# Kernel optimization log

Measured on AMD Instinct MI355X. Metric: run time of the kernel, lower is better.

Reference implementation:

```python
import jax, jax.numpy as jnp
import numpy as np

B, S, D = 4, 2048, 1024
H = 16
DK = D // H  # 64, dim_k == dim_v
FF = 4096
EPS = 1e-5


def layer_norm(x, g, b):
    mu = jnp.mean(x, axis=-1, keepdims=True)
    var = jnp.mean(jnp.square(x - mu), axis=-1, keepdims=True)
    return (x - mu) * jax.lax.rsqrt(var + EPS) * g + b


def setup_inputs() -> dict:
    key = jax.random.key(0)
    ks = jax.random.split(key, 16)
    s = 0.02
    return {
        "src": jax.random.normal(ks[0], (B, S, D), jnp.float32),
        # per-head Q/K/V projections (stacked over heads)
        "wq": jax.random.normal(ks[1], (H, D, DK), jnp.float32) * s,
        "bq": jnp.zeros((H, DK), jnp.float32),
        "wk": jax.random.normal(ks[2], (H, D, DK), jnp.float32) * s,
        "bk": jnp.zeros((H, DK), jnp.float32),
        "wv": jax.random.normal(ks[3], (H, D, DK), jnp.float32) * s,
        "bv": jnp.zeros((H, DK), jnp.float32),
        # output projection: concat(H*DK) -> D
        "wo": jax.random.normal(ks[4], (H * DK, D), jnp.float32) * s,
        "bo": jnp.zeros((D,), jnp.float32),
        "ln1_g": jnp.ones((D,), jnp.float32),
        "ln1_b": jnp.zeros((D,), jnp.float32),
        # FFN
        "w1": jax.random.normal(ks[5], (D, FF), jnp.float32) * s,
        "b1": jnp.zeros((FF,), jnp.float32),
        "w2": jax.random.normal(ks[6], (FF, D), jnp.float32) * s,
        "b2": jnp.zeros((D,), jnp.float32),
        "ln2_g": jnp.ones((D,), jnp.float32),
        "ln2_b": jnp.zeros((D,), jnp.float32),
    }


def reference(src, wq, bq, wk, bk, wv, bv, wo, bo, ln1_g, ln1_b,
              w1, b1, w2, b2, ln2_g, ln2_b):
    # per-head projections: [B,S,D] x [H,D,K] -> [B,H,S,K]
    q = jnp.einsum('bsd,hdk->bhsk', src, wq) + bq[None, :, None, :]
    k = jnp.einsum('bsd,hdk->bhsk', src, wk) + bk[None, :, None, :]
    v = jnp.einsum('bsd,hdk->bhsk', src, wv) + bv[None, :, None, :]
    scale = 1.0 / jnp.sqrt(jnp.float32(DK))
    scores = jnp.einsum('bhsk,bhtk->bhst', q, k) * scale  # [B,H,S,S]
    attn = jax.nn.softmax(scores, axis=-1)
    o = jnp.einsum('bhst,bhtv->bhsv', attn, v)            # [B,H,S,DK]
    o = o.transpose(0, 2, 1, 3).reshape(B, S, H * DK)      # concat heads
    attn_out = o @ wo + bo
    x = layer_norm(src + attn_out, ln1_g, ln1_b)
    ff = jax.nn.relu(x @ w1 + b1) @ w2 + b2
    return layer_norm(x + ff, ln2_g, ln2_b)
```

## Files before the change

kernel.cpp:

```cpp
#include <hip/hip_runtime.h>

typedef __bf16 bf16;
typedef __bf16 bf16x8 __attribute__((ext_vector_type(8)));
typedef __bf16 bf16x4 __attribute__((ext_vector_type(4)));
typedef float  f32x4  __attribute__((ext_vector_type(4)));
typedef float  f32x16 __attribute__((ext_vector_type(16)));
typedef unsigned int u32;
typedef int i32x2 __attribute__((ext_vector_type(2)));

#define NB 4
#define NS 2048
#define ND 1024
#define NH 16
#define NDK 64
#define NFF 4096
#define NM (NB*NS)

#define QSCALE 0.18033688f

__device__ __forceinline__ void load_lds16(const void* g, void* l) {
  __builtin_amdgcn_global_load_lds(
      (const __attribute__((address_space(1))) void*)g,
      (__attribute__((address_space(3))) void*)l, 16, 0, 0);
}

__device__ __forceinline__ u32 pack2(float a, float b) {
  union { bf16 h[2]; u32 u; } z;
  z.h[0] = (bf16)a; z.h[1] = (bf16)b;
  return z.u;
}

__device__ __forceinline__ i32x2 pswap(u32 a, u32 b) {
#if __has_builtin(__builtin_amdgcn_permlane32_swap)
  return __builtin_amdgcn_permlane32_swap((int)a, (int)b, false, false);
#else
  u32 x = a, y = b;
  asm volatile("v_permlane32_swap_b32 %0, %1" : "+v"(x), "+v"(y));
  i32x2 r; r[0] = (int)x; r[1] = (int)y; return r;
#endif
}

__global__ __launch_bounds__(256)
void cvt_f32_bf16(const float* __restrict__ in, bf16* __restrict__ out, int n) {
  int i = (blockIdx.x * 256 + threadIdx.x) * 4;
  if (i < n) {
    float4 v = *(const float4*)&in[i];
    bf16x4 o;
    o[0] = (bf16)v.x; o[1] = (bf16)v.y; o[2] = (bf16)v.z; o[3] = (bf16)v.w;
    *(bf16x4*)&out[i] = o;
  }
}

__global__ __launch_bounds__(256)
void transpose_cvt(const float* __restrict__ in, bf16* __restrict__ out,
                   int R, int C, size_t in_bs, size_t out_bs) {
  __shared__ float t[32][33];
  int bx = blockIdx.x, by = blockIdx.y, bz = blockIdx.z;
  const float* ip = in + (size_t)bz * in_bs + (size_t)(bx * 32) * C + by * 32;
  bf16* op = out + (size_t)bz * out_bs + (size_t)(by * 32) * R + bx * 32;
  int x = threadIdx.x & 31, y = threadIdx.x >> 5;
#pragma unroll
  for (int yy = 0; yy < 32; yy += 8)
    t[y + yy][x] = ip[(size_t)(y + yy) * C + x];
  __syncthreads();
#pragma unroll
  for (int yy = 0; yy < 32; yy += 8)
    op[(size_t)(y + yy) * R + x] = (bf16)t[x][y + yy];
}

__global__ __launch_bounds__(256)
void transpose_v(const bf16* __restrict__ v, bf16* __restrict__ vT) {
  __shared__ bf16 t[64][72];
  int st = blockIdx.x;
  int bh = blockIdx.y;
  const bf16* ip = v + ((size_t)bh * NS + st * 64) * NDK;
  bf16* op = vT + (size_t)bh * NDK * NS + st * 64;
  int tid = threadIdx.x;
#pragma unroll
  for (int c = tid; c < 512; c += 256) {
    int r = c >> 3, q = c & 7;
    bf16x8 d = *(const bf16x8*)&ip[(size_t)r * NDK + q * 8];
#pragma unroll
    for (int j = 0; j < 8; j++) t[r][q * 8 + j] = d[j];
  }
  __syncthreads();
#pragma unroll
  for (int c = tid; c < 512; c += 256) {
    int dv = c >> 3, sq = c & 7;
    bf16x8 d;
#pragma unroll
    for (int j = 0; j < 8; j++) d[j] = t[sq * 8 + j][dv];
    *(bf16x8*)&op[(size_t)dv * NS + sq * 8] = d;
  }
}

#define BAR()  __builtin_amdgcn_s_barrier()
#define LGKM0() do { asm volatile("s_waitcnt lgkmcnt(0)" ::: "memory"); \
                     __builtin_amdgcn_sched_barrier(0); } while (0)

template<int BN, int EPI>
__global__ __launch_bounds__(512, 2)
void gemm8p(const bf16* __restrict__ A, const bf16* __restrict__ Bt,
            const float* __restrict__ bias0, const float* __restrict__ bias1,
            const float* __restrict__ bias2, void* __restrict__ out0,
            int M, int N, int K) {
  constexpr int NFR = BN / 64;
  __shared__ __align__(16) bf16 lA[2][256 * 64];
  __shared__ __align__(16) bf16 lB[2][BN * 64];

  const int tid = threadIdx.x, lane = tid & 63, w = tid >> 6;
  const int wr = w >> 2, wn = w & 3;
  const int blane = lane & 15, glane = lane >> 4;

  const int nwg = gridDim.x;
  const int cpx = nwg >> 3;
  const int bid = blockIdx.x;
  const int swzb = (bid & 7) * cpx + (bid >> 3);
  const int gridM = M >> 8;
  const int bm = (swzb % gridM) * 256;
  const int bn = (swzb / gridM) * BN;

  f32x4 acc[8][NFR] = {};
  bf16x8 aF[8], bF[2 * NFR];

  auto stageA = [&](int kt, int h, int b) {
#pragma unroll
    for (int j = 0; j < 2; j++) {
      int ch = w * 128 + j * 64 + lane;
      int r = h * 128 + (ch >> 3), s = ch & 7;
      load_lds16(A + (size_t)(bm + r) * K + kt * 64 + ((s ^ (r & 7)) * 8),
                 &lA[b][(h * 1024 + ch) * 8]);
    }
  };
  auto stageB = [&](int kt, int h, int b) {
    if constexpr (BN == 256) {
#pragma unroll
      for (int j = 0; j < 2; j++) {
        int ch = w * 128 + j * 64 + lane;
        int r = h * 128 + (ch >> 3), s = ch & 7;
        load_lds16(Bt + (size_t)(bn + r) * K + kt * 64 + ((s ^ (r & 7)) * 8),
                   &lB[b][(h * 1024 + ch) * 8]);
      }
    } else {
      int ch = w * 64 + lane;
      int r = h * 64 + (ch >> 3), s = ch & 7;
      load_lds16(Bt + (size_t)(bn + r) * K + kt * 64 + ((s ^ (r & 7)) * 8),
                 &lB[b][(h * 512 + ch) * 8]);
    }
  };
  auto vmwait = [&]() {
    if constexpr (BN == 256) asm volatile("s_waitcnt vmcnt(6)" ::: "memory");
    else                     asm volatile("s_waitcnt vmcnt(4)" ::: "memory");
  };
  auto ldA = [&](int mh, int b) {
#pragma unroll
    for (int mf = 0; mf < 4; mf++)
#pragma unroll
      for (int ks = 0; ks < 2; ks++) {
        int r = wr * 128 + mh * 64 + mf * 16 + blane;
        int s = (ks * 4 + glane) ^ (r & 7);
        aF[mf * 2 + ks] = *(const bf16x8*)&lA[b][r * 64 + s * 8];
      }
  };
  auto ldBh = [&](int nh, int b) {
#pragma unroll
    for (int nq = 0; nq < NFR / 2; nq++)
#pragma unroll
      for (int ks = 0; ks < 2; ks++) {
        int nf = nh * (NFR / 2) + nq;
        int r = wn * (NFR * 16) + nf * 16 + blane;
        int s = (ks * 4 + glane) ^ (r & 7);
        bF[nf * 2 + ks] = *(const bf16x8*)&lB[b][r * 64 + s * 8];
      }
  };

#define MMAQ(mh, nh)  do {                                                  \
    __builtin_amdgcn_s_setprio(1);                                          \
    _Pragma("unroll")                                                       \
    for (int mf = 0; mf < 4; mf++)                                          \
      _Pragma("unroll")                                                     \
      for (int nq = 0; nq < NFR / 2; nq++)                                  \
        _Pragma("unroll")                                                   \
        for (int ks = 0; ks < 2; ks++)                                      \
          acc[(mh) * 4 + mf][(nh) * (NFR / 2) + nq] =                       \
            __builtin_amdgcn_mfma_f32_16x16x32_bf16(                        \
              aF[mf * 2 + ks], bF[((nh) * (NFR / 2) + nq) * 2 + ks],        \
              acc[(mh) * 4 + mf][(nh) * (NFR / 2) + nq], 0, 0, 0);          \
    __builtin_amdgcn_s_setprio(0);                                          \
  } while (0)

  stageB(0, 0, 0); stageB(0, 1, 0); stageA(0, 0, 0); stageA(0, 1, 0);
  stageB(1, 0, 1); stageB(1, 1, 1); stageA(1, 0, 1);
  vmwait();
  BAR();

  const int NT = K >> 6;
  for (int u = 0; u < NT; u += 2) {
    const int t2 = (u + 2 < NT) ? u + 2 : u;
    const int t3 = (u + 3 < NT) ? u + 3 : u + 1;
    ldA(0, 0); ldBh(0, 0);
    stageA(u + 1, 1, 1);
    BAR(); LGKM0(); MMAQ(0, 0); BAR();
    ldBh(1, 0);
    stageB(t2, 0, 0);
    BAR(); LGKM0(); MMAQ(0, 1); BAR();
    ldA(1, 0);
    stageB(t2, 1, 0);
    BAR(); LGKM0(); MMAQ(1, 1); BAR();
    stageA(t2, 0, 0);
    BAR(); MMAQ(1, 0); vmwait(); BAR();
    ldA(0, 1); ldBh(0, 1);
    stageA(t2, 1, 0);
    BAR(); LGKM0(); MMAQ(0, 0); BAR();
    ldBh(1, 1);
    stageB(t3, 0, 1);
    BAR(); LGKM0(); MMAQ(0, 1); BAR();
    ldA(1, 1);
    stageB(t3, 1, 1);
    BAR(); LGKM0(); MMAQ(1, 1); BAR();
    stageA(t3, 0, 1);
    BAR(); MMAQ(1, 0); vmwait(); BAR();
  }

#pragma unroll
  for (int am = 0; am < 8; am++) {
#pragma unroll
    for (int nf = 0; nf < NFR; nf++) {
      int col = bn + wn * (NFR * 16) + nf * 16 + blane;
      int rowb = bm + wr * 128 + (am >> 2) * 64 + (am & 3) * 16 + glane * 4;
      if (EPI == 0) {
        int sel = col >> 10;
        int hh = (col & 1023) >> 6;
        int dv = col & 63;
        const float* bp = (sel == 0) ? bias0 : (sel == 1) ? bias1 : bias2;
        float bias = bp[col & 1023];
        float sc = (sel == 0) ? QSCALE : 1.0f;
        bf16* outb = (bf16*)out0 + (size_t)sel * NB * NH * NS * NDK;
#pragma unroll
        for (int i = 0; i < 4; i++) {
          int row = rowb + i;
          int b_ = row >> 11, s_ = row & 2047;
          outb[(((size_t)(b_ * NH + hh) * NS + s_) * NDK) + dv] = (bf16)((acc[am][nf][i] + bias) * sc);
        }
      } else if (EPI == 1) {
        float bias = bias0[col];
#pragma unroll
        for (int i = 0; i < 4; i++) {
          float v = acc[am][nf][i] + bias;
          v = v > 0.f ? v : 0.f;
          ((bf16*)out0)[(size_t)(rowb + i) * N + col] = (bf16)v;
        }
      } else {
        float bias = bias0[col];
#pragma unroll
        for (int i = 0; i < 4; i++)
          ((float*)out0)[(size_t)(rowb + i) * N + col] = acc[am][nf][i] + bias;
      }
    }
  }
#undef MMAQ
}

__global__ __launch_bounds__(256)
void flash_attn5(const bf16* __restrict__ q, const bf16* __restrict__ k,
                 const bf16* __restrict__ vT, bf16* __restrict__ o) {
  __shared__ __align__(16) bf16 lK[2][64 * 64];
  __shared__ __align__(16) bf16 lV[2][64 * 64];
  const int tid = threadIdx.x, lane = tid & 63, w = tid >> 6;
  const int ql = lane & 31, hi = lane >> 5;
  const int bh = blockIdx.y, qt = blockIdx.x;
  const size_t hb = (size_t)bh * NS * NDK;
  const int qrow = qt * 128 + w * 32 + ql;

  bf16x8 qf[4];
#pragma unroll
  for (int ks = 0; ks < 4; ks++)
    qf[ks] = *(const bf16x8*)&q[hb + (size_t)qrow * NDK + ks * 16 + hi * 8];

  const int rA = tid & 63;
  const int sA = tid >> 6;
  const bf16* kc0 = k  + hb + (size_t)rA * NDK + sA * 8;
  const bf16* kc1 = k  + hb + (size_t)rA * NDK + (sA + 4) * 8;
  const bf16* vc0 = vT + hb + (size_t)rA * NS  + sA * 8;
  const bf16* vc1 = vT + hb + (size_t)rA * NS  + (sA + 4) * 8;

  f32x16 o0 = {}, o1 = {};
  float ls0 = 0.f, ls1 = 0.f, ls2 = 0.f, ls3 = 0.f;

  load_lds16(kc0, &lK[0][tid * 8]);
  load_lds16(kc1, &lK[0][(tid + 256) * 8]);
  load_lds16(vc0, &lV[0][tid * 8]);
  load_lds16(vc1, &lV[0][(tid + 256) * 8]);
  __syncthreads();

  const char* lKc = (const char*)&lK[0][0];
  const char* lVc = (const char*)&lV[0][0];

  for (int t = 0; t < NS / 64; t++) {
    const int cur = t & 1;
    if (t < NS / 64 - 1) {
      const size_t ko = (size_t)(t + 1) * 64 * NDK;
      const int vo = (t + 1) * 64;
      load_lds16(kc0 + ko, &lK[cur ^ 1][tid * 8]);
      load_lds16(kc1 + ko, &lK[cur ^ 1][(tid + 256) * 8]);
      load_lds16(vc0 + vo, &lV[cur ^ 1][tid * 8]);
      load_lds16(vc1 + vo, &lV[cur ^ 1][(tid + 256) * 8]);
    }
    const char* Kb = lKc + cur * 8192;
    const char* Vb = lVc + cur * 8192;

    f32x16 st0 = {}, st1 = {};
    __builtin_amdgcn_s_setprio(1);
#pragma unroll
    for (int ks = 0; ks < 4; ks++) {
      const int c = 2 * ks + hi;
      bf16x8 kf0 = *(const bf16x8*)(Kb + ((c * 64 + ql) << 4));
      bf16x8 kf1 = *(const bf16x8*)(Kb + ((c * 64 + 32 + ql) << 4));
      st0 = __builtin_amdgcn_mfma_f32_32x32x16_bf16(kf0, qf[ks], st0, 0, 0, 0);
      st1 = __builtin_amdgcn_mfma_f32_32x32x16_bf16(kf1, qf[ks], st1, 0, 0, 0);
    }
    __builtin_amdgcn_s_setprio(0);

#pragma unroll
    for (int r = 0; r < 16; r += 4) {
      float p00 = exp2f(st0[r]),     p01 = exp2f(st0[r + 1]);
      float p02 = exp2f(st0[r + 2]), p03 = exp2f(st0[r + 3]);
      float p10 = exp2f(st1[r]),     p11 = exp2f(st1[r + 1]);
      float p12 = exp2f(st1[r + 2]), p13 = exp2f(st1[r + 3]);
      st0[r] = p00; st0[r + 1] = p01; st0[r + 2] = p02; st0[r + 3] = p03;
      st1[r] = p10; st1[r + 1] = p11; st1[r + 2] = p12; st1[r + 3] = p13;
      ls0 += p00 + p10; ls1 += p01 + p11;
      ls2 += p02 + p12; ls3 += p03 + p13;
    }

#pragma unroll
    for (int tt = 0; tt < 2; tt++) {
      f32x16 stv = (tt == 0) ? st0 : st1;
      u32 wv[8];
#pragma unroll
      for (int i = 0; i < 8; i++) wv[i] = pack2(stv[2 * i], stv[2 * i + 1]);
#pragma unroll
      for (int kk = 0; kk < 2; kk++) {
        const int base = 4 * kk;
        i32x2 e0 = pswap(wv[base + 0], wv[base + 2]);
        i32x2 e1 = pswap(wv[base + 1], wv[base + 3]);
        union { u32 u[4]; bf16x8 v; } pf;
        pf.u[0] = (u32)e0[0];
        pf.u[1] = (u32)e1[0];
        pf.u[2] = (u32)e0[1];
        pf.u[3] = (u32)e1[1];
        const int ks = 2 * tt + kk;
        const int c = 2 * ks + hi;
        bf16x8 vf0 = *(const bf16x8*)(Vb + ((c * 64 + ql) << 4));
        bf16x8 vf1 = *(const bf16x8*)(Vb + ((c * 64 + 32 + ql) << 4));
        __builtin_amdgcn_s_setprio(1);
        o0 = __builtin_amdgcn_mfma_f32_32x32x16_bf16(vf0, pf.v, o0, 0, 0, 0);
        o1 = __builtin_amdgcn_mfma_f32_32x32x16_bf16(vf1, pf.v, o1, 0, 0, 0);
        __builtin_amdgcn_s_setprio(0);
      }
    }
    __syncthreads();
  }

  float ls = (ls0 + ls1) + (ls2 + ls3);
  float lR;
  {
    i32x2 sr = pswap((u32)__float_as_int(ls), (u32)__float_as_int(ls));
    float lsp = __int_as_float(hi ? sr[0] : sr[1]);
    float lo_ = hi ? lsp : ls, hi_ = hi ? ls : lsp;
    lR = lo_ + hi_;
  }
  float invl = 1.0f / lR;
  int b_ = bh >> 4, h_ = bh & 15;
  bf16* ob = o + ((size_t)(b_ * NS + qrow) * (NH * NDK)) + h_ * NDK;
#pragma unroll
  for (int rp = 0; rp < 8; rp++) {
    int dv = 8 * (rp >> 1) + 2 * (rp & 1) + 4 * hi;
    *(u32*)&ob[dv]      = pack2(o0[2 * rp] * invl, o0[2 * rp + 1] * invl);
    *(u32*)&ob[dv + 32] = pack2(o1[2 * rp] * invl, o1[2 * rp + 1] * invl);
  }
}

template<int WB>
__global__ __launch_bounds__(256)
void ln_res(const float* __restrict__ a, const float* __restrict__ b,
            const float* __restrict__ g, const float* __restrict__ be,
            float* __restrict__ y, bf16* __restrict__ yb) {
  int row = blockIdx.x;
  int tid = threadIdx.x;
  const float4* a4 = (const float4*)(a + (size_t)row * ND);
  const float4* b4 = (const float4*)(b + (size_t)row * ND);
  float4 av = a4[tid], bv = b4[tid];
  float x0 = av.x + bv.x, x1 = av.y + bv.y, x2 = av.z + bv.z, x3 = av.w + bv.w;
  float s = x0 + x1 + x2 + x3;
  float qq_ = x0 * x0 + x1 * x1 + x2 * x2 + x3 * x3;
#pragma unroll
  for (int d = 1; d < 64; d <<= 1) { s += __shfl_xor(s, d); qq_ += __shfl_xor(qq_, d); }
  __shared__ float ss[4], sq[4];
  int w = tid >> 6, lane = tid & 63;
  if (lane == 0) { ss[w] = s; sq[w] = qq_; }
  __syncthreads();
  s = ss[0] + ss[1] + ss[2] + ss[3];
  qq_ = sq[0] + sq[1] + sq[2] + sq[3];
  float mu = s * (1.0f / ND);
  float var = qq_ * (1.0f / ND) - mu * mu;
  float rs = 1.0f / sqrtf(var + 1e-5f);
  const float4* g4 = (const float4*)g;
  const float4* e4 = (const float4*)be;
  float4 gv = g4[tid], ev = e4[tid];
  float o0 = (x0 - mu) * rs * gv.x + ev.x;
  float o1 = (x1 - mu) * rs * gv.y + ev.y;
  float o2 = (x2 - mu) * rs * gv.z + ev.z;
  float o3 = (x3 - mu) * rs * gv.w + ev.w;
  float4 ov = {o0, o1, o2, o3};
  *(float4*)(y + (size_t)row * ND + tid * 4) = ov;
  if (WB) {
    bf16x4 wv;
    wv[0] = (bf16)o0; wv[1] = (bf16)o1; wv[2] = (bf16)o2; wv[3] = (bf16)o3;
    *(bf16x4*)&yb[(size_t)row * ND + tid * 4] = wv;
  }
}

extern "C" void kernel_launch(void* const* d_in, const int* in_sizes, int n_in,
                              void* d_out, int out_size, void* d_ws, size_t ws_size,
                              hipStream_t stream) {
  const float* src = (const float*)d_in[0];
  const float* wq  = (const float*)d_in[1];
  const float* bq  = (const float*)d_in[2];
  const float* wk  = (const float*)d_in[3];
  const float* bk  = (const float*)d_in[4];
  const float* wv  = (const float*)d_in[5];
  const float* bv  = (const float*)d_in[6];
  const float* wo  = (const float*)d_in[7];
  const float* bo  = (const float*)d_in[8];
  const float* g1  = (const float*)d_in[9];
  const float* be1 = (const float*)d_in[10];
  const float* w1  = (const float*)d_in[11];
  const float* b1  = (const float*)d_in[12];
  const float* w2  = (const float*)d_in[13];
  const float* b2  = (const float*)d_in[14];
  const float* g2  = (const float*)d_in[15];
  const float* be2 = (const float*)d_in[16];

  char* ws = (char*)d_ws;
  bf16*  srcb  = (bf16*)(ws + 0);
  bf16*  wqkvT = (bf16*)(ws + 16777216);
  bf16*  woT   = (bf16*)(ws + 23068672);
  bf16*  w1T   = (bf16*)(ws + 25165824);
  bf16*  w2T   = (bf16*)(ws + 33554432);
  bf16*  qkv   = (bf16*)(ws + 41943040);
  bf16*  vT    = (bf16*)(ws + 92274688);
  bf16*  attno = (bf16*)(ws + 109051904);
  float* tmpf  = (float*)(ws + 125829120);
  float* x     = (float*)(ws + 159383552);
  bf16*  xb    = (bf16*)(ws + 192937984);
  bf16*  hbuf  = qkv;

  const size_t QKVSZ = (size_t)NB * NH * NS * NDK;

  cvt_f32_bf16<<<8192, 256, 0, stream>>>(src, srcb, NM * ND);
  transpose_cvt<<<dim3(32, 2, 16), 256, 0, stream>>>(wq, wqkvT,               1024, 64, 65536, 65536);
  transpose_cvt<<<dim3(32, 2, 16), 256, 0, stream>>>(wk, wqkvT + 1024 * 1024, 1024, 64, 65536, 65536);
  transpose_cvt<<<dim3(32, 2, 16), 256, 0, stream>>>(wv, wqkvT + 2048 * 1024, 1024, 64, 65536, 65536);
  transpose_cvt<<<dim3(32, 32, 1), 256, 0, stream>>>(wo, woT, 1024, 1024, 0, 0);
  transpose_cvt<<<dim3(32, 128, 1), 256, 0, stream>>>(w1, w1T, 1024, 4096, 0, 0);
  transpose_cvt<<<dim3(128, 32, 1), 256, 0, stream>>>(w2, w2T, 4096, 1024, 0, 0);

  gemm8p<256, 0><<<384, 512, 0, stream>>>(srcb, wqkvT, bq, bk, bv, qkv, NM, 3072, 1024);
  transpose_v<<<dim3(32, 64), 256, 0, stream>>>(qkv + 2 * QKVSZ, vT);
  flash_attn5<<<dim3(16, 64), 256, 0, stream>>>(qkv, qkv + QKVSZ, vT, attno);
  gemm8p<128, 2><<<256, 512, 0, stream>>>(attno, woT, bo, nullptr, nullptr, tmpf, NM, 1024, 1024);
  ln_res<1><<<8192, 256, 0, stream>>>(src, tmpf, g1, be1, x, xb);
  gemm8p<256, 1><<<512, 512, 0, stream>>>(xb, w1T, b1, nullptr, nullptr, hbuf, NM, 4096, 1024);
  gemm8p<128, 2><<<256, 512, 0, stream>>>(hbuf, w2T, b2, nullptr, nullptr, tmpf, NM, 1024, 4096);
  ln_res<0><<<8192, 256, 0, stream>>>(x, tmpf, g2, be2, (float*)d_out, nullptr);
}
```

Before: 501.4 us.

## Swizzle flash-attention K/V LDS layout and remap blocks to XCDs per head

After: 486.6 us. -2.9%, faster.

```diff
diff --git a/kernel.cpp b/kernel.cpp
--- a/kernel.cpp
+++ b/kernel.cpp
@@ -262,13 +262,18 @@
 }
 
 __global__ __launch_bounds__(256)
-void flash_attn5(const bf16* __restrict__ q, const bf16* __restrict__ k,
+void flash_attn6(const bf16* __restrict__ q, const bf16* __restrict__ k,
                  const bf16* __restrict__ vT, bf16* __restrict__ o) {
   __shared__ __align__(16) bf16 lK[2][64 * 64];
   __shared__ __align__(16) bf16 lV[2][64 * 64];
   const int tid = threadIdx.x, lane = tid & 63, w = tid >> 6;
   const int ql = lane & 31, hi = lane >> 5;
-  const int bh = blockIdx.y, qt = blockIdx.x;
+
+  const int id = blockIdx.x;
+  const int xcd = id & 7, sseq = id >> 3;
+  const int bh = xcd * 8 + (sseq >> 4);
+  const int qt = sseq & 15;
+
   const size_t hb = (size_t)bh * NS * NDK;
   const int qrow = qt * 128 + w * 32 + ql;
 
@@ -277,34 +282,35 @@
   for (int ks = 0; ks < 4; ks++)
     qf[ks] = *(const bf16x8*)&q[hb + (size_t)qrow * NDK + ks * 16 + hi * 8];
 
-  const int rA = tid & 63;
-  const int sA = tid >> 6;
-  const bf16* kc0 = k  + hb + (size_t)rA * NDK + sA * 8;
-  const bf16* kc1 = k  + hb + (size_t)rA * NDK + (sA + 4) * 8;
-  const bf16* vc0 = vT + hb + (size_t)rA * NS  + sA * 8;
-  const bf16* vc1 = vT + hb + (size_t)rA * NS  + (sA + 4) * 8;
+  const int r0 = tid >> 3, s0 = ((tid & 7) ^ (r0 & 7)) * 8;
+  const int r1 = r0 + 32, s1 = ((tid & 7) ^ (r1 & 7)) * 8;
+  const bf16* k0 = k + hb + (size_t)r0 * NDK + s0;
+  const bf16* k1 = k + hb + (size_t)r1 * NDK + s1;
+  const bf16* v0 = vT + hb + (size_t)r0 * NS + s0;
+  const bf16* v1 = vT + hb + (size_t)r1 * NS + s1;
 
   f32x16 o0 = {}, o1 = {};
   float ls0 = 0.f, ls1 = 0.f, ls2 = 0.f, ls3 = 0.f;
 
-  load_lds16(kc0, &lK[0][tid * 8]);
-  load_lds16(kc1, &lK[0][(tid + 256) * 8]);
-  load_lds16(vc0, &lV[0][tid * 8]);
-  load_lds16(vc1, &lV[0][(tid + 256) * 8]);
+  load_lds16(k0, &lK[0][tid * 8]);
+  load_lds16(k1, &lK[0][(tid + 256) * 8]);
+  load_lds16(v0, &lV[0][tid * 8]);
+  load_lds16(v1, &lV[0][(tid + 256) * 8]);
   __syncthreads();
 
   const char* lKc = (const char*)&lK[0][0];
   const char* lVc = (const char*)&lV[0][0];
+  const int swz = (ql & 7) << 4;
 
   for (int t = 0; t < NS / 64; t++) {
     const int cur = t & 1;
     if (t < NS / 64 - 1) {
       const size_t ko = (size_t)(t + 1) * 64 * NDK;
       const int vo = (t + 1) * 64;
-      load_lds16(kc0 + ko, &lK[cur ^ 1][tid * 8]);
-      load_lds16(kc1 + ko, &lK[cur ^ 1][(tid + 256) * 8]);
-      load_lds16(vc0 + vo, &lV[cur ^ 1][tid * 8]);
-      load_lds16(vc1 + vo, &lV[cur ^ 1][(tid + 256) * 8]);
+      load_lds16(k0 + ko, &lK[cur ^ 1][tid * 8]);
+      load_lds16(k1 + ko, &lK[cur ^ 1][(tid + 256) * 8]);
+      load_lds16(v0 + vo, &lV[cur ^ 1][tid * 8]);
+      load_lds16(v1 + vo, &lV[cur ^ 1][(tid + 256) * 8]);
     }
     const char* Kb = lKc + cur * 8192;
     const char* Vb = lVc + cur * 8192;
@@ -313,9 +319,9 @@
     __builtin_amdgcn_s_setprio(1);
 #pragma unroll
     for (int ks = 0; ks < 4; ks++) {
-      const int c = 2 * ks + hi;
-      bf16x8 kf0 = *(const bf16x8*)(Kb + ((c * 64 + ql) << 4));
-      bf16x8 kf1 = *(const bf16x8*)(Kb + ((c * 64 + 32 + ql) << 4));
+      int byt = (32 * ks + 16 * hi) ^ swz;
+      bf16x8 kf0 = *(const bf16x8*)(Kb + ql * 128 + byt);
+      bf16x8 kf1 = *(const bf16x8*)(Kb + (32 + ql) * 128 + byt);
       st0 = __builtin_amdgcn_mfma_f32_32x32x16_bf16(kf0, qf[ks], st0, 0, 0, 0);
       st1 = __builtin_amdgcn_mfma_f32_32x32x16_bf16(kf1, qf[ks], st1, 0, 0, 0);
     }
@@ -350,9 +356,9 @@
         pf.u[2] = (u32)e0[1];
         pf.u[3] = (u32)e1[1];
         const int ks = 2 * tt + kk;
-        const int c = 2 * ks + hi;
-        bf16x8 vf0 = *(const bf16x8*)(Vb + ((c * 64 + ql) << 4));
-        bf16x8 vf1 = *(const bf16x8*)(Vb + ((c * 64 + 32 + ql) << 4));
+        int vbyt = (32 * ks + 16 * hi) ^ swz;
+        bf16x8 vf0 = *(const bf16x8*)(Vb + ql * 128 + vbyt);
+        bf16x8 vf1 = *(const bf16x8*)(Vb + (32 + ql) * 128 + vbyt);
         __builtin_amdgcn_s_setprio(1);
         o0 = __builtin_amdgcn_mfma_f32_32x32x16_bf16(vf0, pf.v, o0, 0, 0, 0);
         o1 = __builtin_amdgcn_mfma_f32_32x32x16_bf16(vf1, pf.v, o1, 0, 0, 0);
@@ -468,7 +474,7 @@
 
   gemm8p<256, 0><<<384, 512, 0, stream>>>(srcb, wqkvT, bq, bk, bv, qkv, NM, 3072, 1024);
   transpose_v<<<dim3(32, 64), 256, 0, stream>>>(qkv + 2 * QKVSZ, vT);
-  flash_attn5<<<dim3(16, 64), 256, 0, stream>>>(qkv, qkv + QKVSZ, vT, attno);
+  flash_attn6<<<1024, 256, 0, stream>>>(qkv, qkv + QKVSZ, vT, attno);
   gemm8p<128, 2><<<256, 512, 0, stream>>>(attno, woT, bo, nullptr, nullptr, tmpf, NM, 1024, 1024);
   ln_res<1><<<8192, 256, 0, stream>>>(src, tmpf, g1, be1, x, xb);
   gemm8p<256, 1><<<512, 512, 0, stream>>>(xb, w1T, b1, nullptr, nullptr, hbuf, NM, 4096, 1024);
```
